# Kernel tuning notes

Measured on AMD Instinct MI355X. Metric: run time of the kernel, lower is better.

## Reference

```python
import jax, jax.numpy as jnp
import numpy as np

B, I, H = 64, 1024, 1024

def _linear_params(key, fan_in, fan_out):
    kw, kb = jax.random.split(key)
    bound = 1.0 / np.sqrt(fan_in)
    W = jax.random.uniform(kw, (fan_in, fan_out), minval=-bound, maxval=bound, dtype=jnp.float32)
    b = jax.random.uniform(kb, (fan_out,), minval=-bound, maxval=bound, dtype=jnp.float32)
    return W, b

def setup_inputs() -> dict:
    key = jax.random.key(0)
    ks = jax.random.split(key, 12)
    Wi, bi = _linear_params(ks[0], I + H, H)
    Wf, bf = _linear_params(ks[1], I + H, H)
    Wo, bo = _linear_params(ks[2], I + H, H)
    Wk, bk = _linear_params(ks[3], I, H)
    Wv, bv = _linear_params(ks[4], I, H)
    Wq, bq = _linear_params(ks[5], H, H)
    We, be = _linear_params(ks[6], H, H)
    x = jax.random.normal(ks[7], (B, I), dtype=jnp.float32)
    h_prev = jax.random.normal(ks[8], (B, H), dtype=jnp.float32)
    C_prev = jax.random.normal(ks[9], (B, H, H), dtype=jnp.float32)
    n_prev = jnp.ones((B, H), dtype=jnp.float32)
    return {"x": x, "h_prev": h_prev, "C_prev": C_prev, "n_prev": n_prev,
            "Wi": Wi, "bi": bi, "Wf": Wf, "bf": bf, "Wo": Wo, "bo": bo,
            "Wk": Wk, "bk": bk, "Wv": Wv, "bv": bv, "Wq": Wq, "bq": bq,
            "We": We, "be": be}

def reference(x, h_prev, C_prev, n_prev, Wi, bi, Wf, bf, Wo, bo, Wk, bk, Wv, bv, Wq, bq, We, be):
    combined = jnp.concatenate([x, h_prev], axis=1)            # [B, I+H]
    i_t = jax.nn.sigmoid(combined @ Wi + bi)                   # [B, H]
    f_t = jax.nn.sigmoid(combined @ Wf + bf)
    o_t = jax.nn.sigmoid(combined @ Wo + bo)
    k_t = x @ Wk + bk                                          # [B, H]
    v_t = x @ Wv + bv
    q_t = h_prev @ Wq + bq
    # outer-product memory update: C_t[b] = f*C_prev[b] + i*(v_t[b] ⊗ k_t[b])
    C_t = f_t[:, :, None] * C_prev + i_t[:, :, None] * jnp.einsum('bi,bj->bij', v_t, k_t)
    n_t = f_t * n_prev + i_t * jnp.exp(k_t @ We + be)
    h_t = o_t * (jnp.einsum('bij,bj->bi', C_t, q_t) / n_t)
    return (h_t, C_t, n_t)
```

## Files before the change

### kernel.cpp

```cpp
#include <hip/hip_runtime.h>
#include <math.h>

#define Bn 64
#define Hn 1024
#define BH 65536

#define WS_GP (6 * BH)
#define WS_NP (30 * BH)

__global__ __launch_bounds__(256) void gates_partial(
    const float* __restrict__ x, const float* __restrict__ h_prev,
    const float* __restrict__ Wi, const float* __restrict__ Wf,
    const float* __restrict__ Wo, const float* __restrict__ Wk,
    const float* __restrict__ Wv, const float* __restrict__ Wq,
    float* __restrict__ ws)
{
    const int g = blockIdx.z, s = blockIdx.y;
    const float* Wm;
    int Ktot;
    switch (g) {
        case 0: Wm = Wi; Ktot = 2048; break;
        case 1: Wm = Wf; Ktot = 2048; break;
        case 2: Wm = Wo; Ktot = 2048; break;
        case 3: Wm = Wk; Ktot = 1024; break;
        case 4: Wm = Wv; Ktot = 1024; break;
        default: Wm = Wq; Ktot = 1024; break;
    }
    const int chunk = Ktot >> 2;
    const int kbase = s * chunk;

    __shared__ float A_lds[64][64];

    const int t  = threadIdx.x;
    const int n0 = (blockIdx.x << 6) + (t & 31);
    const int n1 = n0 + 32;
    const int rg = t >> 5;

    float acc0[8], acc1[8];
    #pragma unroll
    for (int r = 0; r < 8; ++r) { acc0[r] = 0.f; acc1[r] = 0.f; }

    for (int kc = 0; kc < chunk; kc += 64) {
        const int k0 = kbase + kc;
        const float* Ab;
        int kloc;
        if (g < 3)       { Ab = (k0 < 1024) ? x : h_prev; kloc = k0 & 1023; }
        else if (g == 5) { Ab = h_prev; kloc = k0; }
        else             { Ab = x;      kloc = k0; }

        __syncthreads();
        {
            const int c     = (t & 15) << 2;
            const int rbase = t >> 4;
            #pragma unroll
            for (int rr = 0; rr < 4; ++rr) {
                const int row = rbase + (rr << 4);
                *(float4*)&A_lds[row][c] =
                    *(const float4*)&Ab[(size_t)row * 1024 + kloc + c];
            }
        }
        __syncthreads();

        #pragma unroll 4
        for (int kk = 0; kk < 64; kk += 4) {
            const size_t wb = (size_t)(k0 + kk) * 1024;
            const float w00 = Wm[wb          + n0], w01 = Wm[wb          + n1];
            const float w10 = Wm[wb + 1024   + n0], w11 = Wm[wb + 1024   + n1];
            const float w20 = Wm[wb + 2048   + n0], w21 = Wm[wb + 2048   + n1];
            const float w30 = Wm[wb + 3072   + n0], w31 = Wm[wb + 3072   + n1];
            #pragma unroll
            for (int r = 0; r < 8; ++r) {
                const float4 a = *(const float4*)&A_lds[rg * 8 + r][kk];
                acc0[r] += a.x * w00 + a.y * w10 + a.z * w20 + a.w * w30;
                acc1[r] += a.x * w01 + a.y * w11 + a.z * w21 + a.w * w31;
            }
        }
    }

    float* P = ws + WS_GP + (size_t)(g * 4 + s) * BH;
    #pragma unroll
    for (int r = 0; r < 8; ++r) {
        const int row = rg * 8 + r;
        P[(size_t)row * 1024 + n0] = acc0[r];
        P[(size_t)row * 1024 + n1] = acc1[r];
    }
}

__global__ __launch_bounds__(256) void gates_finalize(
    const float* __restrict__ bi, const float* __restrict__ bf,
    const float* __restrict__ bo, const float* __restrict__ bk,
    const float* __restrict__ bv, const float* __restrict__ bq,
    float* __restrict__ ws)
{
    const int id = blockIdx.x * 256 + threadIdx.x;
    const int g  = id >> 16;
    const int r  = id & 0xFFFF;
    const int n  = r & 1023;
    const float* P = ws + WS_GP + (size_t)g * 4 * BH;
    float v = P[r] + P[BH + r] + P[2 * BH + r] + P[3 * BH + r];
    const float* bias;
    switch (g) {
        case 0: bias = bi; break; case 1: bias = bf; break;
        case 2: bias = bo; break; case 3: bias = bk; break;
        case 4: bias = bv; break; default: bias = bq; break;
    }
    v += bias[n];
    if (g < 3) v = 1.f / (1.f + expf(-v));
    ws[(size_t)g * BH + r] = v;
}

__global__ __launch_bounds__(256) void ngate_partial(
    const float* __restrict__ We, const float* __restrict__ ws_in,
    float* __restrict__ ws)
{
    const int s = blockIdx.y;
    const int chunk = 256;
    const int kbase = s * chunk;
    const float* kt = ws_in + 3 * BH;

    __shared__ float A_lds[64][64];

    const int t  = threadIdx.x;
    const int n0 = (blockIdx.x << 6) + (t & 31);
    const int n1 = n0 + 32;
    const int rg = t >> 5;

    float acc0[8], acc1[8];
    #pragma unroll
    for (int r = 0; r < 8; ++r) { acc0[r] = 0.f; acc1[r] = 0.f; }

    for (int kc = 0; kc < chunk; kc += 64) {
        const int k0 = kbase + kc;
        __syncthreads();
        {
            const int c     = (t & 15) << 2;
            const int rbase = t >> 4;
            #pragma unroll
            for (int rr = 0; rr < 4; ++rr) {
                const int row = rbase + (rr << 4);
                *(float4*)&A_lds[row][c] =
                    *(const float4*)&kt[(size_t)row * 1024 + k0 + c];
            }
        }
        __syncthreads();

        #pragma unroll 4
        for (int kk = 0; kk < 64; kk += 4) {
            const size_t wb = (size_t)(k0 + kk) * 1024;
            const float w00 = We[wb          + n0], w01 = We[wb          + n1];
            const float w10 = We[wb + 1024   + n0], w11 = We[wb + 1024   + n1];
            const float w20 = We[wb + 2048   + n0], w21 = We[wb + 2048   + n1];
            const float w30 = We[wb + 3072   + n0], w31 = We[wb + 3072   + n1];
            #pragma unroll
            for (int r = 0; r < 8; ++r) {
                const float4 a = *(const float4*)&A_lds[rg * 8 + r][kk];
                acc0[r] += a.x * w00 + a.y * w10 + a.z * w20 + a.w * w30;
                acc1[r] += a.x * w01 + a.y * w11 + a.z * w21 + a.w * w31;
            }
        }
    }

    float* P = ws + WS_NP + (size_t)s * BH;
    #pragma unroll
    for (int r = 0; r < 8; ++r) {
        const int row = rg * 8 + r;
        P[(size_t)row * 1024 + n0] = acc0[r];
        P[(size_t)row * 1024 + n1] = acc1[r];
    }
}

__global__ __launch_bounds__(256) void ngate_finalize(
    const float* __restrict__ be, const float* __restrict__ n_prev,
    const float* __restrict__ ws, float* __restrict__ n_out)
{
    const int id = blockIdx.x * 256 + threadIdx.x;
    const float* P = ws + WS_NP;
    const float m = P[id] + P[BH + id] + P[2 * BH + id] + P[3 * BH + id]
                  + be[id & 1023];
    n_out[id] = ws[BH + id] * n_prev[id] + ws[id] * expf(m);
}

__global__ __launch_bounds__(256) void c_update(
    const float* __restrict__ C_prev, const float* __restrict__ ws,
    const float* __restrict__ n_t, float* __restrict__ h_t,
    float* __restrict__ C_t)
{
    const int t    = threadIdx.x;
    const int lane = t & 63;
    const int w    = t >> 6;
    const int R0   = blockIdx.x * 32 + w * 8;
    const int b    = R0 >> 10;

    const float4* kp = (const float4*)(ws + 3 * BH + (size_t)b * 1024);
    const float4* qp = (const float4*)(ws + 5 * BH + (size_t)b * 1024);
    float4 k4[4], q4[4];
    #pragma unroll
    for (int c = 0; c < 4; ++c) {
        k4[c] = kp[c * 64 + lane];
        q4[c] = qp[c * 64 + lane];
    }

    #pragma unroll 2
    for (int r = 0; r < 8; ++r) {
        const int R    = R0 + r;
        const float f  = ws[1 * BH + R];
        const float iv = ws[0 * BH + R] * ws[4 * BH + R];
        const float4* cp = (const float4*)(C_prev + (size_t)R * 1024);
        float4*       co = (float4*)(C_t + (size_t)R * 1024);

        float dot = 0.f;
        #pragma unroll
        for (int c = 0; c < 4; ++c) {
            const float4 c4 = cp[c * 64 + lane];
            float4 o4;
            o4.x = f * c4.x + iv * k4[c].x;
            o4.y = f * c4.y + iv * k4[c].y;
            o4.z = f * c4.z + iv * k4[c].z;
            o4.w = f * c4.w + iv * k4[c].w;
            co[c * 64 + lane] = o4;
            dot += o4.x * q4[c].x + o4.y * q4[c].y
                 + o4.z * q4[c].z + o4.w * q4[c].w;
        }
        #pragma unroll
        for (int off = 32; off; off >>= 1)
            dot += __shfl_xor(dot, off);
        if (lane == 0)
            h_t[R] = ws[2 * BH + R] * dot / n_t[R];
    }
}

extern "C" void kernel_launch(void* const* d_in, const int* in_sizes, int n_in,
                              void* d_out, int out_size, void* d_ws, size_t ws_size,
                              hipStream_t stream)
{
    const float* x      = (const float*)d_in[0];
    const float* h_prev = (const float*)d_in[1];
    const float* C_prev = (const float*)d_in[2];
    const float* n_prev = (const float*)d_in[3];
    const float* Wi = (const float*)d_in[4];  const float* bi = (const float*)d_in[5];
    const float* Wf = (const float*)d_in[6];  const float* bf = (const float*)d_in[7];
    const float* Wo = (const float*)d_in[8];  const float* bo = (const float*)d_in[9];
    const float* Wk = (const float*)d_in[10]; const float* bk = (const float*)d_in[11];
    const float* Wv = (const float*)d_in[12]; const float* bv = (const float*)d_in[13];
    const float* Wq = (const float*)d_in[14]; const float* bq = (const float*)d_in[15];
    const float* We = (const float*)d_in[16]; const float* be = (const float*)d_in[17];

    float* out = (float*)d_out;
    float* h_t = out;
    float* C_t = out + BH;
    float* n_t = out + BH + (size_t)Bn * Hn * Hn;
    float* ws  = (float*)d_ws;

    gates_partial<<<dim3(16, 4, 6), 256, 0, stream>>>(
        x, h_prev, Wi, Wf, Wo, Wk, Wv, Wq, ws);

    gates_finalize<<<(6 * BH) / 256, 256, 0, stream>>>(
        bi, bf, bo, bk, bv, bq, ws);

    ngate_partial<<<dim3(16, 4), 256, 0, stream>>>(We, ws, ws);

    ngate_finalize<<<BH / 256, 256, 0, stream>>>(be, n_prev, ws, n_t);

    c_update<<<2048, 256, 0, stream>>>(C_prev, ws, n_t, h_t, C_t);
}
```

Before: 633.6 us.

## Increase split-K, vectorize GEMM tiles, fuse n-gate finalize into C update

```diff
diff --git a/kernel.cpp b/kernel.cpp
--- a/kernel.cpp
+++ b/kernel.cpp
@@ -5,8 +5,10 @@
 #define Hn 1024
 #define BH 65536
 
+typedef float v4f __attribute__((ext_vector_type(4)));
+
 #define WS_GP (6 * BH)
-#define WS_NP (30 * BH)
+#define WS_NP (54 * BH)
 
 __global__ __launch_bounds__(256) void gates_partial(
     const float* __restrict__ x, const float* __restrict__ h_prev,
@@ -26,19 +28,19 @@
         case 4: Wm = Wv; Ktot = 1024; break;
         default: Wm = Wq; Ktot = 1024; break;
     }
-    const int chunk = Ktot >> 2;
+    const int chunk = Ktot >> 3;
     const int kbase = s * chunk;
 
-    __shared__ float A_lds[64][64];
+    __shared__ float A_lds[64][68];
 
     const int t  = threadIdx.x;
-    const int n0 = (blockIdx.x << 6) + (t & 31);
-    const int n1 = n0 + 32;
-    const int rg = t >> 5;
-
-    float acc0[8], acc1[8];
-    #pragma unroll
-    for (int r = 0; r < 8; ++r) { acc0[r] = 0.f; acc1[r] = 0.f; }
+    const int cg = t & 15;
+    const int rg = t >> 4;
+    const int n0 = (blockIdx.x << 6) + (cg << 2);
+
+    float4 acc[4];
+    #pragma unroll
+    for (int r = 0; r < 4; ++r) acc[r] = make_float4(0.f, 0.f, 0.f, 0.f);
 
     for (int kc = 0; kc < chunk; kc += 64) {
         const int k0 = kbase + kc;
@@ -50,40 +52,38 @@
 
         __syncthreads();
         {
-            const int c     = (t & 15) << 2;
-            const int rbase = t >> 4;
+            const int c = cg << 2;
             #pragma unroll
             for (int rr = 0; rr < 4; ++rr) {
-                const int row = rbase + (rr << 4);
+                const int row = rg + (rr << 4);
                 *(float4*)&A_lds[row][c] =
                     *(const float4*)&Ab[(size_t)row * 1024 + kloc + c];
             }
         }
         __syncthreads();
 
-        #pragma unroll 4
+        #pragma unroll 2
         for (int kk = 0; kk < 64; kk += 4) {
-            const size_t wb = (size_t)(k0 + kk) * 1024;
-            const float w00 = Wm[wb          + n0], w01 = Wm[wb          + n1];
-            const float w10 = Wm[wb + 1024   + n0], w11 = Wm[wb + 1024   + n1];
-            const float w20 = Wm[wb + 2048   + n0], w21 = Wm[wb + 2048   + n1];
-            const float w30 = Wm[wb + 3072   + n0], w31 = Wm[wb + 3072   + n1];
+            const float* wp = Wm + (size_t)(k0 + kk) * 1024 + n0;
+            const float4 w0 = *(const float4*)(wp);
+            const float4 w1 = *(const float4*)(wp + 1024);
+            const float4 w2 = *(const float4*)(wp + 2048);
+            const float4 w3 = *(const float4*)(wp + 3072);
             #pragma unroll
-            for (int r = 0; r < 8; ++r) {
-                const float4 a = *(const float4*)&A_lds[rg * 8 + r][kk];
-                acc0[r] += a.x * w00 + a.y * w10 + a.z * w20 + a.w * w30;
-                acc1[r] += a.x * w01 + a.y * w11 + a.z * w21 + a.w * w31;
+            for (int r = 0; r < 4; ++r) {
+                const float4 a = *(const float4*)&A_lds[(rg << 2) + r][kk];
+                acc[r].x += a.x * w0.x + a.y * w1.x + a.z * w2.x + a.w * w3.x;
+                acc[r].y += a.x * w0.y + a.y * w1.y + a.z * w2.y + a.w * w3.y;
+                acc[r].z += a.x * w0.z + a.y * w1.z + a.z * w2.z + a.w * w3.z;
+                acc[r].w += a.x * w0.w + a.y * w1.w + a.z * w2.w + a.w * w3.w;
             }
         }
     }
 
-    float* P = ws + WS_GP + (size_t)(g * 4 + s) * BH;
-    #pragma unroll
-    for (int r = 0; r < 8; ++r) {
-        const int row = rg * 8 + r;
-        P[(size_t)row * 1024 + n0] = acc0[r];
-        P[(size_t)row * 1024 + n1] = acc1[r];
-    }
+    float* P = ws + WS_GP + (size_t)(g * 8 + s) * BH;
+    #pragma unroll
+    for (int r = 0; r < 4; ++r)
+        *(float4*)&P[(size_t)((rg << 2) + r) * 1024 + n0] = acc[r];
 }
 
 __global__ __launch_bounds__(256) void gates_finalize(
@@ -92,98 +92,90 @@
     const float* __restrict__ bv, const float* __restrict__ bq,
     float* __restrict__ ws)
 {
-    const int id = blockIdx.x * 256 + threadIdx.x;
-    const int g  = id >> 16;
-    const int r  = id & 0xFFFF;
-    const int n  = r & 1023;
-    const float* P = ws + WS_GP + (size_t)g * 4 * BH;
-    float v = P[r] + P[BH + r] + P[2 * BH + r] + P[3 * BH + r];
+    const int v4 = blockIdx.x * 256 + threadIdx.x;
+    const int g  = v4 >> 14;
+    const int r4 = v4 & 16383;
+    const float4* P = (const float4*)(ws + WS_GP + (size_t)g * 8 * BH);
+    float4 a = P[r4];
+    #pragma unroll
+    for (int s = 1; s < 8; ++s) {
+        const float4 p = P[(size_t)s * (BH / 4) + r4];
+        a.x += p.x; a.y += p.y; a.z += p.z; a.w += p.w;
+    }
     const float* bias;
     switch (g) {
         case 0: bias = bi; break; case 1: bias = bf; break;
         case 2: bias = bo; break; case 3: bias = bk; break;
         case 4: bias = bv; break; default: bias = bq; break;
     }
-    v += bias[n];
-    if (g < 3) v = 1.f / (1.f + expf(-v));
-    ws[(size_t)g * BH + r] = v;
+    const float4 b4 = ((const float4*)bias)[r4 & 255];
+    a.x += b4.x; a.y += b4.y; a.z += b4.z; a.w += b4.w;
+    if (g < 3) {
+        a.x = 1.f / (1.f + expf(-a.x));
+        a.y = 1.f / (1.f + expf(-a.y));
+        a.z = 1.f / (1.f + expf(-a.z));
+        a.w = 1.f / (1.f + expf(-a.w));
+    }
+    ((float4*)ws)[v4] = a;
 }
 
 __global__ __launch_bounds__(256) void ngate_partial(
-    const float* __restrict__ We, const float* __restrict__ ws_in,
-    float* __restrict__ ws)
-{
-    const int s = blockIdx.y;
-    const int chunk = 256;
-    const int kbase = s * chunk;
-    const float* kt = ws_in + 3 * BH;
-
-    __shared__ float A_lds[64][64];
+    const float* __restrict__ We, float* __restrict__ ws)
+{
+    const int s  = blockIdx.y;
+    const int k0 = s * 64;
+    const float* kt = ws + 3 * BH;
+
+    __shared__ float A_lds[64][68];
 
     const int t  = threadIdx.x;
-    const int n0 = (blockIdx.x << 6) + (t & 31);
-    const int n1 = n0 + 32;
-    const int rg = t >> 5;
-
-    float acc0[8], acc1[8];
-    #pragma unroll
-    for (int r = 0; r < 8; ++r) { acc0[r] = 0.f; acc1[r] = 0.f; }
-
-    for (int kc = 0; kc < chunk; kc += 64) {
-        const int k0 = kbase + kc;
-        __syncthreads();
-        {
-            const int c     = (t & 15) << 2;
-            const int rbase = t >> 4;
-            #pragma unroll
-            for (int rr = 0; rr < 4; ++rr) {
-                const int row = rbase + (rr << 4);
-                *(float4*)&A_lds[row][c] =
-                    *(const float4*)&kt[(size_t)row * 1024 + k0 + c];
-            }
-        }
-        __syncthreads();
-
-        #pragma unroll 4
-        for (int kk = 0; kk < 64; kk += 4) {
-            const size_t wb = (size_t)(k0 + kk) * 1024;
-            const float w00 = We[wb          + n0], w01 = We[wb          + n1];
-            const float w10 = We[wb + 1024   + n0], w11 = We[wb + 1024   + n1];
-            const float w20 = We[wb + 2048   + n0], w21 = We[wb + 2048   + n1];
-            const float w30 = We[wb + 3072   + n0], w31 = We[wb + 3072   + n1];
-            #pragma unroll
-            for (int r = 0; r < 8; ++r) {
-                const float4 a = *(const float4*)&A_lds[rg * 8 + r][kk];
-                acc0[r] += a.x * w00 + a.y * w10 + a.z * w20 + a.w * w30;
-                acc1[r] += a.x * w01 + a.y * w11 + a.z * w21 + a.w * w31;
-            }
+    const int cg = t & 15;
+    const int rg = t >> 4;
+    const int n0 = (blockIdx.x << 6) + (cg << 2);
+
+    float4 acc[4];
+    #pragma unroll
+    for (int r = 0; r < 4; ++r) acc[r] = make_float4(0.f, 0.f, 0.f, 0.f);
+
+    {
+        const int c = cg << 2;
+        #pragma unroll
+        for (int rr = 0; rr < 4; ++rr) {
+            const int row = rg + (rr << 4);
+            *(float4*)&A_lds[row][c] =
+                *(const float4*)&kt[(size_t)row * 1024 + k0 + c];
+        }
+    }
+    __syncthreads();
+
+    #pragma unroll 2
+    for (int kk = 0; kk < 64; kk += 4) {
+        const float* wp = We + (size_t)(k0 + kk) * 1024 + n0;
+        const float4 w0 = *(const float4*)(wp);
+        const float4 w1 = *(const float4*)(wp + 1024);
+        const float4 w2 = *(const float4*)(wp + 2048);
+        const float4 w3 = *(const float4*)(wp + 3072);
+        #pragma unroll
+        for (int r = 0; r < 4; ++r) {
+            const float4 a = *(const float4*)&A_lds[(rg << 2) + r][kk];
+            acc[r].x += a.x * w0.x + a.y * w1.x + a.z * w2.x + a.w * w3.x;
+            acc[r].y += a.x * w0.y + a.y * w1.y + a.z * w2.y + a.w * w3.y;
+            acc[r].z += a.x * w0.z + a.y * w1.z + a.z * w2.z + a.w * w3.z;
+            acc[r].w += a.x * w0.w + a.y * w1.w + a.z * w2.w + a.w * w3.w;
         }
     }
 
     float* P = ws + WS_NP + (size_t)s * BH;
     #pragma unroll
-    for (int r = 0; r < 8; ++r) {
-        const int row = rg * 8 + r;
-        P[(size_t)row * 1024 + n0] = acc0[r];
-        P[(size_t)row * 1024 + n1] = acc1[r];
-    }
-}
-
-__global__ __launch_bounds__(256) void ngate_finalize(
-    const float* __restrict__ be, const float* __restrict__ n_prev,
-    const float* __restrict__ ws, float* __restrict__ n_out)
-{
-    const int id = blockIdx.x * 256 + threadIdx.x;
-    const float* P = ws + WS_NP;
-    const float m = P[id] + P[BH + id] + P[2 * BH + id] + P[3 * BH + id]
-                  + be[id & 1023];
-    n_out[id] = ws[BH + id] * n_prev[id] + ws[id] * expf(m);
+    for (int r = 0; r < 4; ++r)
+        *(float4*)&P[(size_t)((rg << 2) + r) * 1024 + n0] = acc[r];
 }
 
 __global__ __launch_bounds__(256) void c_update(
     const float* __restrict__ C_prev, const float* __restrict__ ws,
-    const float* __restrict__ n_t, float* __restrict__ h_t,
-    float* __restrict__ C_t)
+    const float* __restrict__ be, const float* __restrict__ n_prev,
+    float* __restrict__ h_t, float* __restrict__ C_t,
+    float* __restrict__ n_out)
 {
     const int t    = threadIdx.x;
     const int lane = t & 63;
@@ -204,28 +196,37 @@
     for (int r = 0; r < 8; ++r) {
         const int R    = R0 + r;
         const float f  = ws[1 * BH + R];
-        const float iv = ws[0 * BH + R] * ws[4 * BH + R];
-        const float4* cp = (const float4*)(C_prev + (size_t)R * 1024);
-        float4*       co = (float4*)(C_t + (size_t)R * 1024);
+        const float i_ = ws[0 * BH + R];
+        const float iv = i_ * ws[4 * BH + R];
+
+        float m = be[R & 1023];
+        #pragma unroll
+        for (int s = 0; s < 16; ++s) m += ws[WS_NP + (size_t)s * BH + R];
+        const float n = f * n_prev[R] + i_ * expf(m);
+
+        const v4f* cp = (const v4f*)(C_prev + (size_t)R * 1024);
+        v4f*       co = (v4f*)(C_t + (size_t)R * 1024);
 
         float dot = 0.f;
         #pragma unroll
         for (int c = 0; c < 4; ++c) {
-            const float4 c4 = cp[c * 64 + lane];
-            float4 o4;
+            const v4f c4 = __builtin_nontemporal_load(&cp[c * 64 + lane]);
+            v4f o4;
             o4.x = f * c4.x + iv * k4[c].x;
             o4.y = f * c4.y + iv * k4[c].y;
             o4.z = f * c4.z + iv * k4[c].z;
             o4.w = f * c4.w + iv * k4[c].w;
-            co[c * 64 + lane] = o4;
+            __builtin_nontemporal_store(o4, &co[c * 64 + lane]);
             dot += o4.x * q4[c].x + o4.y * q4[c].y
                  + o4.z * q4[c].z + o4.w * q4[c].w;
         }
         #pragma unroll
         for (int off = 32; off; off >>= 1)
             dot += __shfl_xor(dot, off);
-        if (lane == 0)
-            h_t[R] = ws[2 * BH + R] * dot / n_t[R];
+        if (lane == 0) {
+            h_t[R]   = ws[2 * BH + R] * dot / n;
+            n_out[R] = n;
+        }
     }
 }
 
@@ -251,15 +252,14 @@
     float* n_t = out + BH + (size_t)Bn * Hn * Hn;
     float* ws  = (float*)d_ws;
 
-    gates_partial<<<dim3(16, 4, 6), 256, 0, stream>>>(
+    gates_partial<<<dim3(16, 8, 6), 256, 0, stream>>>(
         x, h_prev, Wi, Wf, Wo, Wk, Wv, Wq, ws);
 
-    gates_finalize<<<(6 * BH) / 256, 256, 0, stream>>>(
+    gates_finalize<<<384, 256, 0, stream>>>(
         bi, bf, bo, bk, bv, bq, ws);
 
-    ngate_partial<<<dim3(16, 4), 256, 0, stream>>>(We, ws, ws);
-
-    ngate_finalize<<<BH / 256, 256, 0, stream>>>(be, n_prev, ws, n_t);
-
-    c_update<<<2048, 256, 0, stream>>>(C_prev, ws, n_t, h_t, C_t);
-}
+    ngate_partial<<<dim3(16, 16), 256, 0, stream>>>(We, ws);
+
+    c_update<<<2048, 256, 0, stream>>>(
+        C_prev, ws, be, n_prev, h_t, C_t, n_t);
+}
```

New measurement: 521.5 us. 17.7% less time.
